# Optimization experiments

Measured on AMD Instinct MI355X. Metric: run time of the kernel, lower is better.

Reference implementation:

```python
import jax, jax.numpy as jnp
import numpy as np

N_FINE = 50000
N_COARSE = 2000
N_EDGES = 300000
HID = 512
OUT = 3
K = 3


def _gcn_prep(edge_index, n):
    # PyG GCNConv with add_self_loops=True, improved=False, edge_weight=1
    row, col = edge_index[0], edge_index[1]
    loop = jnp.arange(n, dtype=edge_index.dtype)
    row = jnp.concatenate([row, loop])
    col = jnp.concatenate([col, loop])
    deg = jax.ops.segment_sum(jnp.ones(row.shape[0], dtype=jnp.float32), col, num_segments=n)
    dis = jax.lax.rsqrt(deg)  # deg >= 1 due to self loops
    norm = dis[row] * dis[col]
    return row, col, norm


def _gcn(h, W, b, row, col, norm, n):
    # linear -> gather source -> weight by norm -> scatter-add at target -> +bias
    h = h @ W
    msg = h[row] * norm[:, None]
    return jax.ops.segment_sum(msg, col, num_segments=n) + b


def _knn_interpolate(y, coarse_pos, fine_pos, k=K):
    # squared euclidean distances [N_fine, N_coarse]
    d2 = (jnp.sum(fine_pos * fine_pos, axis=1, keepdims=True)
          + jnp.sum(coarse_pos * coarse_pos, axis=1)[None, :]
          - 2.0 * fine_pos @ coarse_pos.T)
    neg, idx = jax.lax.top_k(-d2, k)          # k nearest
    w = 1.0 / jnp.maximum(-neg, 1e-16)        # inverse squared-distance weights
    return jnp.einsum('nk,nkc->nc', w, y[idx]) / jnp.sum(w, axis=1, keepdims=True)


def setup_inputs() -> dict:
    key = jax.random.key(0)
    ks = jax.random.split(key, 20)
    x = jax.random.normal(ks[0], (N_FINE, 5), dtype=jnp.float32)
    sdf = jax.random.normal(ks[1], (N_FINE, 1), dtype=jnp.float32)
    edge_index = jax.random.randint(ks[2], (2, N_EDGES), 0, N_FINE)
    coarse_x = jax.random.normal(ks[3], (N_COARSE, 2), dtype=jnp.float32)
    coarse_y = jax.random.normal(ks[4], (N_COARSE, OUT), dtype=jnp.float32)
    dims_pre = [(6, HID), (HID, HID), (HID, HID)]
    dims_end = [(OUT + HID, HID), (HID, HID), (HID, OUT)]
    out = {"x": x, "sdf": sdf, "coarse_x": coarse_x, "coarse_y": coarse_y,
           "edge_index": edge_index}
    for i, (di, do) in enumerate(dims_pre):
        out[f"pre_W{i}"] = jax.random.normal(ks[5 + i], (di, do), dtype=jnp.float32) / np.float32(np.sqrt(di))
        out[f"pre_b{i}"] = jnp.zeros((do,), dtype=jnp.float32)
    for i, (di, do) in enumerate(dims_end):
        out[f"end_W{i}"] = jax.random.normal(ks[10 + i], (di, do), dtype=jnp.float32) / np.float32(np.sqrt(di))
        out[f"end_b{i}"] = jnp.zeros((do,), dtype=jnp.float32)
    return out


def reference(x, sdf, coarse_x, coarse_y, edge_index,
              pre_W0, pre_b0, pre_W1, pre_b1, pre_W2, pre_b2,
              end_W0, end_b0, end_W1, end_b1, end_W2, end_b2):
    n = x.shape[0]
    row, col, norm = _gcn_prep(edge_index, n)

    fine_x = jnp.concatenate([x, sdf], axis=1)  # [N, 6]
    for W, b in ((pre_W0, pre_b0), (pre_W1, pre_b1), (pre_W2, pre_b2)):
        fine_x = jax.nn.relu(_gcn(fine_x, W, b, row, col, norm, n))

    # coarse -> fine KNN upsample (batch.x[:, :2] are fine node positions)
    fine_y_orig = _knn_interpolate(coarse_y, coarse_x[:, :2], x[:, :2])  # [N, 3]

    fine_y = jnp.concatenate([fine_y_orig, fine_x], axis=1)  # [N, 515]
    for W, b in ((end_W0, end_b0), (end_W1, end_b1)):
        fine_y = jax.nn.relu(_gcn(fine_y, W, b, row, col, norm, n))
    fine_y = _gcn(fine_y, end_W2, end_b2, row, col, norm, n)
    return fine_y  # residual=False
```

## Files before the change

kernel.cpp:

```cpp
#include <hip/hip_runtime.h>
#include <hip/hip_bf16.h>

#define N_FINE 50000
#define N_COARSE 2000
#define N_EDGES 300000

typedef short  s16x8 __attribute__((ext_vector_type(8)));
typedef float  f32x4 __attribute__((ext_vector_type(4)));

static inline int cdiv(int a, int b) { return (a + b - 1) / b; }

__device__ __forceinline__ short f2b(float f) {
    unsigned u = __builtin_bit_cast(unsigned, f);
    unsigned r = (u + 0x7fffu + ((u >> 16) & 1u)) >> 16;
    return (short)r;
}
__device__ __forceinline__ float b2f(short s) {
    return __builtin_bit_cast(float, ((unsigned)(unsigned short)s) << 16);
}

#define GL16(gsrc, ldst) __builtin_amdgcn_global_load_lds( \
    (const __attribute__((address_space(1))) unsigned*)(gsrc), \
    (__attribute__((address_space(3))) unsigned*)(ldst), 16, 0, 0)


__global__ void count_edges_kernel(const int* __restrict__ col, int* __restrict__ counts, int ne) {
    int e = blockIdx.x * 256 + threadIdx.x;
    if (e < ne) atomicAdd(&counts[col[e]], 1);
}

__global__ void compute_dis_kernel(const int* __restrict__ counts, float* __restrict__ dis, int n) {
    int i = blockIdx.x * 256 + threadIdx.x;
    if (i < n) dis[i] = rsqrtf((float)(counts[i] + 1));
}

__global__ __launch_bounds__(1024) void scan_block_kernel(const int* __restrict__ counts,
        int* __restrict__ rowptr, int* __restrict__ blksum, int n) {
    __shared__ int wsum[16];
    int tid = threadIdx.x, lane = tid & 63, wv = tid >> 6;
    int i = blockIdx.x * 1024 + tid;
    int v = (i < n) ? counts[i] : 0;
    int x = v;
#pragma unroll
    for (int off = 1; off < 64; off <<= 1) {
        int t = __shfl_up(x, off);
        if (lane >= off) x += t;
    }
    if (lane == 63) wsum[wv] = x;
    __syncthreads();
    if (wv == 0) {
        int s = (lane < 16) ? wsum[lane] : 0;
#pragma unroll
        for (int off = 1; off < 16; off <<= 1) {
            int t = __shfl_up(s, off);
            if (lane >= off) s += t;
        }
        if (lane < 16) wsum[lane] = s;
    }
    __syncthreads();
    int prefix = (wv > 0) ? wsum[wv - 1] : 0;
    int incl = prefix + x;
    if (i < n) rowptr[i] = incl - v;
    if (tid == 1023) blksum[blockIdx.x] = incl;
}

__global__ void scan_tops_kernel(int* __restrict__ blksum, int nb) {
    int lane = threadIdx.x;
    int v = (lane < nb) ? blksum[lane] : 0;
    int x = v;
#pragma unroll
    for (int off = 1; off < 64; off <<= 1) {
        int t = __shfl_up(x, off);
        if (lane >= off) x += t;
    }
    if (lane < nb) blksum[lane] = x - v;
}

__global__ void scan_add_kernel(int* __restrict__ rowptr, const int* __restrict__ blksum, int n) {
    int i = blockIdx.x * 256 + threadIdx.x;
    if (i < n) rowptr[i] += blksum[i >> 10];
    else if (i == n) rowptr[n] = N_EDGES;
}

__global__ void scatter_edges_kernel(const int* __restrict__ row, const int* __restrict__ col,
                                     int* __restrict__ cursor, int* __restrict__ esrc, int ne) {
    int e = blockIdx.x * 256 + threadIdx.x;
    if (e < ne) {
        int p = atomicAdd(&cursor[col[e]], 1);
        esrc[p] = row[e];
    }
}


__global__ __launch_bounds__(256) void wt4_kernel(
        const float* __restrict__ W0, const float* __restrict__ W1,
        const float* __restrict__ W2, const float* __restrict__ W3,
        short* __restrict__ T0, short* __restrict__ T1,
        short* __restrict__ T2, short* __restrict__ T3) {
    __shared__ float tile[32][33];
    const float* W; short* WT;
    switch (blockIdx.y) {
        case 0: W = W0; WT = T0; break;
        case 1: W = W1; WT = T1; break;
        case 2: W = W2; WT = T2; break;
        default: W = W3; WT = T3; break;
    }
    int bx = blockIdx.x & 15;
    int by = blockIdx.x >> 4;
    int tx = threadIdx.x & 31;
    int ty = threadIdx.x >> 5;
#pragma unroll
    for (int i = 0; i < 4; ++i) {
        int k = bx * 32 + ty + i * 8;
        int n = by * 32 + tx;
        tile[ty + i * 8][tx] = W[(size_t)k * 512 + n];
    }
    __syncthreads();
#pragma unroll
    for (int i = 0; i < 4; ++i) {
        int n = by * 32 + ty + i * 8;
        int k = bx * 32 + tx;
        WT[(size_t)n * 512 + k] = f2b(tile[tx][ty + i * 8]);
    }
}


__global__ void pre0_kernel(const float* __restrict__ x, const float* __restrict__ sdf,
                            const float* __restrict__ W, const float* __restrict__ dis,
                            short* __restrict__ B, int M) {
    int idx = blockIdx.x * 256 + threadIdx.x;
    int m = idx >> 6, n8 = (idx & 63) << 3;
    if (m >= M) return;
    float a0 = x[m*5+0], a1 = x[m*5+1], a2 = x[m*5+2], a3 = x[m*5+3], a4 = x[m*5+4], a5 = sdf[m];
    float d = dis[m];
    s16x8 o;
#pragma unroll
    for (int j = 0; j < 8; ++j) {
        int n = n8 + j;
        float t = a0*W[n] + a1*W[512+n] + a2*W[1024+n] + a3*W[1536+n] + a4*W[2048+n] + a5*W[2560+n];
        o[j] = f2b(d * t);
    }
    *(s16x8*)&B[(size_t)m*512 + n8] = o;
}

__global__ __launch_bounds__(256) void gemm512_mfma_kernel(
        const short* __restrict__ A, const short* __restrict__ WT,
        const float* __restrict__ dis, short* __restrict__ C, int M,
        const float* __restrict__ A2, const float* __restrict__ W2) {
    __shared__ __attribute__((aligned(16))) short As[3][128 * 32];
    __shared__ __attribute__((aligned(16))) short Bs[3][128 * 32];
    int tid  = threadIdx.x;
    int lane = tid & 63;
    int w    = tid >> 6;
    int wr   = w >> 1, wc = w & 1;

    int nrp = (M + 127) >> 7;
    int id = blockIdx.x;
    int rp = (id >> 5) * 8 + (id & 7);
    int cp = (id >> 3) & 3;
    if (rp >= nrp) return;
    int row0 = rp * 128;
    int col0 = cp * 128;

    const short* aRow[2];
    const short* bRow[2];
    int ldsOff[2];
#pragma unroll
    for (int g = 0; g < 2; ++g) {
        int r = w * 32 + g * 16 + (lane >> 2);
        int ar = row0 + r; if (ar >= M) ar = M - 1;
        int sch = (lane & 3) ^ ((r >> 1) & 3);
        aRow[g] = A  + (size_t)ar * 512 + sch * 8;
        bRow[g] = WT + (size_t)(col0 + r) * 512 + sch * 8;
        ldsOff[g] = (w * 32 + g * 16) * 32;
    }

    int ks = lane >> 4;
    int aOff[4], bOff[4];
#pragma unroll
    for (int mi = 0; mi < 4; ++mi) {
        int r = wr * 64 + mi * 16 + (lane & 15);
        aOff[mi] = r * 32 + ((ks ^ ((r >> 1) & 3)) * 8);
    }
#pragma unroll
    for (int ni = 0; ni < 4; ++ni) {
        int c = wc * 64 + ni * 16 + (lane & 15);
        bOff[ni] = c * 32 + ((ks ^ ((c >> 1) & 3)) * 8);
    }

    f32x4 acc[4][4] = {};

    auto stage = [&](int buf, int k0) {
#pragma unroll
        for (int g = 0; g < 2; ++g) {
            GL16(aRow[g] + k0, &As[buf][ldsOff[g]]);
            GL16(bRow[g] + k0, &Bs[buf][ldsOff[g]]);
        }
    };
    auto compute = [&](int buf) {
        s16x8 av[4], bv[4];
#pragma unroll
        for (int mi = 0; mi < 4; ++mi) av[mi] = *(const s16x8*)&As[buf][aOff[mi]];
#pragma unroll
        for (int ni = 0; ni < 4; ++ni) bv[ni] = *(const s16x8*)&Bs[buf][bOff[ni]];
#pragma unroll
        for (int mi = 0; mi < 4; ++mi)
#pragma unroll
            for (int ni = 0; ni < 4; ++ni)
                acc[mi][ni] = __builtin_amdgcn_mfma_f32_16x16x32_bf16(av[mi], bv[ni], acc[mi][ni], 0, 0, 0);
    };

    stage(0, 0);
    stage(1, 32);
    int buf = 0;
#pragma unroll 1
    for (int t = 0; t < 16; ++t) {
        if (t + 2 < 16) {
            int b2 = buf + 2; if (b2 >= 3) b2 -= 3;
            stage(b2, (t + 2) * 32);
            asm volatile("s_waitcnt vmcnt(8)" ::: "memory");
        } else if (t + 1 < 16) {
            asm volatile("s_waitcnt vmcnt(4)" ::: "memory");
        } else {
            asm volatile("s_waitcnt vmcnt(0)" ::: "memory");
        }
        __builtin_amdgcn_s_barrier();
        __builtin_amdgcn_sched_barrier(0);
        compute(buf);
        __builtin_amdgcn_sched_barrier(0);
        __builtin_amdgcn_s_barrier();
        __builtin_amdgcn_sched_barrier(0);
        ++buf; if (buf == 3) buf = 0;
    }

    int rbase = row0 + wr * 64;
    int cbase = col0 + wc * 64;
#pragma unroll
    for (int mi = 0; mi < 4; ++mi) {
#pragma unroll
        for (int r = 0; r < 4; ++r) {
            int row = rbase + mi * 16 + (lane >> 4) * 4 + r;
            if (row >= M) continue;
            float d = dis[row];
            float a20 = 0.f, a21 = 0.f, a22 = 0.f;
            if (A2) { a20 = A2[row*3+0]; a21 = A2[row*3+1]; a22 = A2[row*3+2]; }
#pragma unroll
            for (int ni = 0; ni < 4; ++ni) {
                int col = cbase + ni * 16 + (lane & 15);
                float v = acc[mi][ni][r];
                if (A2) v += a20 * W2[col] + a21 * W2[512 + col] + a22 * W2[1024 + col];
                C[(size_t)row * 512 + col] = f2b(d * v);
            }
        }
    }
}

__global__ __launch_bounds__(256) void spmm512_kernel(
        const short* __restrict__ B, const int* __restrict__ rowptr, const int* __restrict__ esrc,
        const float* __restrict__ dis, const float* __restrict__ bias,
        short* __restrict__ out, int M) {
    int node = blockIdx.x * 4 + (threadIdx.x >> 6);
    int lane = threadIdx.x & 63;
    if (node >= M) return;
    const s16x8* Bv = (const s16x8*)B;
    s16x8 v = Bv[(size_t)node * 64 + lane];
    float acc[8];
#pragma unroll
    for (int j = 0; j < 8; ++j) acc[j] = b2f(v[j]);
    int s = rowptr[node], e = rowptr[node + 1];
    int p = s;
    for (; p + 4 <= e; p += 4) {
        int s0 = esrc[p], s1 = esrc[p+1], s2 = esrc[p+2], s3 = esrc[p+3];
        s16x8 t0 = Bv[(size_t)s0 * 64 + lane];
        s16x8 t1 = Bv[(size_t)s1 * 64 + lane];
        s16x8 t2 = Bv[(size_t)s2 * 64 + lane];
        s16x8 t3 = Bv[(size_t)s3 * 64 + lane];
#pragma unroll
        for (int j = 0; j < 8; ++j)
            acc[j] += (b2f(t0[j]) + b2f(t1[j])) + (b2f(t2[j]) + b2f(t3[j]));
    }
    for (; p < e; ++p) {
        int src = esrc[p];
        s16x8 t = Bv[(size_t)src * 64 + lane];
#pragma unroll
        for (int j = 0; j < 8; ++j) acc[j] += b2f(t[j]);
    }
    float d = dis[node];
    const float4* bp = (const float4*)bias;
    float4 bb0 = bp[lane * 2], bb1 = bp[lane * 2 + 1];
    float r[8];
    r[0] = d*acc[0] + bb0.x; r[1] = d*acc[1] + bb0.y; r[2] = d*acc[2] + bb0.z; r[3] = d*acc[3] + bb0.w;
    r[4] = d*acc[4] + bb1.x; r[5] = d*acc[5] + bb1.y; r[6] = d*acc[6] + bb1.z; r[7] = d*acc[7] + bb1.w;
    s16x8 o;
#pragma unroll
    for (int j = 0; j < 8; ++j) o[j] = f2b(fmaxf(r[j], 0.f));
    ((s16x8*)out)[(size_t)node * 64 + lane] = o;
}

__global__ __launch_bounds__(256) void gemm_n3_kernel(
        const short* __restrict__ A, const float* __restrict__ W,
        const float* __restrict__ dis, float* __restrict__ B3, int M) {
    int wid = (blockIdx.x * 256 + threadIdx.x) >> 6;
    int lane = threadIdx.x & 63;
    if (wid >= M) return;
    s16x8 v = ((const s16x8*)A)[(size_t)wid * 64 + lane];
    float s0 = 0.f, s1 = 0.f, s2 = 0.f;
#pragma unroll
    for (int j = 0; j < 8; ++j) {
        float a = b2f(v[j]);
        int k = lane * 8 + j;
        s0 += a * W[k*3+0];
        s1 += a * W[k*3+1];
        s2 += a * W[k*3+2];
    }
    for (int off = 32; off > 0; off >>= 1) {
        s0 += __shfl_down(s0, off);
        s1 += __shfl_down(s1, off);
        s2 += __shfl_down(s2, off);
    }
    if (lane == 0) {
        float d = dis[wid];
        B3[wid*3+0] = d * s0;
        B3[wid*3+1] = d * s1;
        B3[wid*3+2] = d * s2;
    }
}

__global__ void spmm3_kernel(const float* __restrict__ B3, const int* __restrict__ rowptr,
                             const int* __restrict__ esrc, const float* __restrict__ dis,
                             const float* __restrict__ bias, float* __restrict__ out, int M) {
    int i = blockIdx.x * 256 + threadIdx.x;
    if (i >= M) return;
    float a0 = B3[i*3+0], a1 = B3[i*3+1], a2 = B3[i*3+2];
    int s = rowptr[i], e = rowptr[i + 1];
    for (int p = s; p < e; ++p) {
        int src = esrc[p];
        a0 += B3[src*3+0];
        a1 += B3[src*3+1];
        a2 += B3[src*3+2];
    }
    float d = dis[i];
    out[i*3+0] = d * a0 + bias[0];
    out[i*3+1] = d * a1 + bias[1];
    out[i*3+2] = d * a2 + bias[2];
}

__global__ __launch_bounds__(256) void knn_kernel(
        const float* __restrict__ x, const float* __restrict__ cpos,
        const float* __restrict__ cy, float* __restrict__ fy, int M) {
    __shared__ float sd[12][64];
    __shared__ int   si[12][64];
    int lane = threadIdx.x & 63;
    int w = threadIdx.x >> 6;
    int gi = blockIdx.x * 64 + lane;
    int i = (gi < M) ? gi : (M - 1);
    float px = x[i*5+0], py = x[i*5+1];
    float pn2 = px*px + py*py;
    float d0 = 3.0e38f, d1 = 3.0e38f, d2 = 3.0e38f;
    int i0 = 0x7fffffff, i1 = 0x7fffffff, i2 = 0x7fffffff;
    int c0 = w * (N_COARSE / 4), c1 = c0 + (N_COARSE / 4);
    for (int c = c0; c < c1; ++c) {
        float a = cpos[c*2+0], b = cpos[c*2+1];
        float sn2 = a*a + b*b;
        float d = pn2 + sn2 - 2.f * (px * a + py * b);
        if (d < d2) {
            if (d < d1) {
                d2 = d1; i2 = i1;
                if (d < d0) { d1 = d0; i1 = i0; d0 = d; i0 = c; }
                else       { d1 = d;  i1 = c; }
            } else { d2 = d; i2 = c; }
        }
    }
    sd[w*3+0][lane] = d0; si[w*3+0][lane] = i0;
    sd[w*3+1][lane] = d1; si[w*3+1][lane] = i1;
    sd[w*3+2][lane] = d2; si[w*3+2][lane] = i2;
    __syncthreads();
    if (w != 0 || gi >= M) return;
    float cd[12]; int ci[12];
#pragma unroll
    for (int q = 0; q < 12; ++q) { cd[q] = sd[q][lane]; ci[q] = si[q][lane]; }
    float bd[3]; int bi[3];
#pragma unroll
    for (int s = 0; s < 3; ++s) {
        float best = 3.4e38f; int besti = 0x7fffffff; int bq = 0;
#pragma unroll
        for (int q = 0; q < 12; ++q) {
            bool better = (cd[q] < best) || (cd[q] == best && ci[q] < besti);
            if (better) { best = cd[q]; besti = ci[q]; bq = q; }
        }
        bd[s] = best; bi[s] = besti;
        cd[bq] = 3.4e38f; ci[bq] = 0x7fffffff;
    }
    float w0 = 1.f / fmaxf(bd[0], 1e-16f);
    float w1 = 1.f / fmaxf(bd[1], 1e-16f);
    float w2 = 1.f / fmaxf(bd[2], 1e-16f);
    float ws = w0 + w1 + w2;
    int j0 = bi[0], j1 = bi[1], j2 = bi[2];
#pragma unroll
    for (int j = 0; j < 3; ++j) {
        float v = w0 * cy[j0*3+j] + w1 * cy[j1*3+j] + w2 * cy[j2*3+j];
        fy[gi*3+j] = v / ws;
    }
}


extern "C" void kernel_launch(void* const* d_in, const int* in_sizes, int n_in,
                              void* d_out, int out_size, void* d_ws, size_t ws_size,
                              hipStream_t stream) {
    const float* x        = (const float*)d_in[0];
    const float* sdf      = (const float*)d_in[1];
    const float* coarse_x = (const float*)d_in[2];
    const float* coarse_y = (const float*)d_in[3];
    const int*   eidx     = (const int*)d_in[4];
    const float* pre_W0   = (const float*)d_in[5];
    const float* pre_b0   = (const float*)d_in[6];
    const float* pre_W1   = (const float*)d_in[7];
    const float* pre_b1   = (const float*)d_in[8];
    const float* pre_W2   = (const float*)d_in[9];
    const float* pre_b2   = (const float*)d_in[10];
    const float* end_W0   = (const float*)d_in[11];
    const float* end_b0   = (const float*)d_in[12];
    const float* end_W1   = (const float*)d_in[13];
    const float* end_b1   = (const float*)d_in[14];
    const float* end_W2   = (const float*)d_in[15];
    const float* end_b2   = (const float*)d_in[16];
    float* out = (float*)d_out;

    const int M = N_FINE, NE = N_EDGES;
    const int* erow = eidx;
    const int* ecol = eidx + NE;

    char* base = (char*)d_ws;
    size_t off = 0;
    auto alloc = [&](size_t bytes) { char* p = base + off; off = (off + bytes + 255) & ~(size_t)255; return p; };
    int*   counts = (int*)  alloc((size_t)M * 4);
    int*   rowptr = (int*)  alloc((size_t)(M + 1) * 4);
    int*   cursor = (int*)  alloc((size_t)M * 4);
    int*   esrc   = (int*)  alloc((size_t)NE * 4);
    int*   blksum = (int*)  alloc((size_t)64 * 4);
    float* dis    = (float*)alloc((size_t)M * 4);
    float* fy     = (float*)alloc((size_t)M * 3 * 4);
    float* B3     = (float*)alloc((size_t)M * 3 * 4);
    short* WT1    = (short*)alloc((size_t)512 * 512 * 2);
    short* WT2    = (short*)alloc((size_t)512 * 512 * 2);
    short* WT3    = (short*)alloc((size_t)512 * 512 * 2);
    short* WT4    = (short*)alloc((size_t)512 * 512 * 2);
    short* bufA   = (short*)alloc((size_t)M * 512 * 2);
    short* bufB   = (short*)alloc((size_t)M * 512 * 2);
    (void)ws_size;

    wt4_kernel<<<dim3(256, 4), 256, 0, stream>>>(pre_W1, pre_W2, end_W0 + 3 * 512, end_W1,
                                                 WT1, WT2, WT3, WT4);

    hipMemsetAsync(counts, 0, (size_t)M * 4, stream);
    count_edges_kernel<<<cdiv(NE, 256), 256, 0, stream>>>(ecol, counts, NE);
    compute_dis_kernel<<<cdiv(M, 256), 256, 0, stream>>>(counts, dis, M);
    int nb = cdiv(M, 1024);
    scan_block_kernel<<<nb, 1024, 0, stream>>>(counts, rowptr, blksum, M);
    scan_tops_kernel<<<1, 64, 0, stream>>>(blksum, nb);
    scan_add_kernel<<<cdiv(M + 1, 256), 256, 0, stream>>>(rowptr, blksum, M);
    hipMemcpyAsync(cursor, rowptr, (size_t)M * 4, hipMemcpyDeviceToDevice, stream);
    scatter_edges_kernel<<<cdiv(NE, 256), 256, 0, stream>>>(erow, ecol, cursor, esrc, NE);

    knn_kernel<<<cdiv(M, 64), 256, 0, stream>>>(x, coarse_x, coarse_y, fy, M);

    int nrp = cdiv(M, 128);
    int ggrid = cdiv(nrp, 8) * 32;
    int sgrid = cdiv(M, 4);

    pre0_kernel<<<cdiv(M * 64, 256), 256, 0, stream>>>(x, sdf, pre_W0, dis, bufB, M);
    spmm512_kernel<<<sgrid, 256, 0, stream>>>(bufB, rowptr, esrc, dis, pre_b0, bufA, M);

    gemm512_mfma_kernel<<<ggrid, 256, 0, stream>>>(bufA, WT1, dis, bufB, M, nullptr, nullptr);
    spmm512_kernel<<<sgrid, 256, 0, stream>>>(bufB, rowptr, esrc, dis, pre_b1, bufA, M);

    gemm512_mfma_kernel<<<ggrid, 256, 0, stream>>>(bufA, WT2, dis, bufB, M, nullptr, nullptr);
    spmm512_kernel<<<sgrid, 256, 0, stream>>>(bufB, rowptr, esrc, dis, pre_b2, bufA, M);

    gemm512_mfma_kernel<<<ggrid, 256, 0, stream>>>(bufA, WT3, dis, bufB, M, fy, end_W0);
    spmm512_kernel<<<sgrid, 256, 0, stream>>>(bufB, rowptr, esrc, dis, end_b0, bufA, M);

    gemm512_mfma_kernel<<<ggrid, 256, 0, stream>>>(bufA, WT4, dis, bufB, M, nullptr, nullptr);
    spmm512_kernel<<<sgrid, 256, 0, stream>>>(bufB, rowptr, esrc, dis, end_b1, bufA, M);

    gemm_n3_kernel<<<cdiv(M * 64, 256), 256, 0, stream>>>(bufA, end_W2, dis, B3, M);
    spmm3_kernel<<<cdiv(M, 256), 256, 0, stream>>>(B3, rowptr, esrc, dis, end_b2, out, M);
}
```

Measured before the change: 680.2 us.

## Enlarge MFMA GEMM tile to 256x128 with 8 waves and BK=64 pipeline

The 512-wide bf16 GEMM now uses 512-thread blocks computing 256x128 output tiles with a K-step of 64. The A tile is triple-buffered and the B tile double-buffered in LDS, with an XOR swizzle adapted to 64-wide rows. Global-to-LDS loads for the next steps are issued between the two K-halves of each step, and the MFMA bursts are wrapped in s_setprio. This raises per-block data reuse and overlaps loads with compute, at the cost of about 128 KB of LDS per block, which limits occupancy to one block per CU.

```diff
diff --git a/kernel.cpp b/kernel.cpp
--- a/kernel.cpp
+++ b/kernel.cpp
@@ -143,98 +143,113 @@
     *(s16x8*)&B[(size_t)m*512 + n8] = o;
 }
 
-__global__ __launch_bounds__(256) void gemm512_mfma_kernel(
+__global__ __launch_bounds__(512) void gemm512_mfma_kernel(
         const short* __restrict__ A, const short* __restrict__ WT,
         const float* __restrict__ dis, short* __restrict__ C, int M,
         const float* __restrict__ A2, const float* __restrict__ W2) {
-    __shared__ __attribute__((aligned(16))) short As[3][128 * 32];
-    __shared__ __attribute__((aligned(16))) short Bs[3][128 * 32];
+    __shared__ __attribute__((aligned(16))) short As[3 * 256 * 64];
+    __shared__ __attribute__((aligned(16))) short Bs[2 * 128 * 64];
     int tid  = threadIdx.x;
     int lane = tid & 63;
     int w    = tid >> 6;
-    int wr   = w >> 1, wc = w & 1;
-
-    int nrp = (M + 127) >> 7;
+    int wm   = w >> 1, wn = w & 1;
+
+    int nrp = (M + 255) >> 8;
     int id = blockIdx.x;
     int rp = (id >> 5) * 8 + (id & 7);
     int cp = (id >> 3) & 3;
     if (rp >= nrp) return;
-    int row0 = rp * 128;
+    int row0 = rp * 256;
     int col0 = cp * 128;
 
-    const short* aRow[2];
-    const short* bRow[2];
-    int ldsOff[2];
-#pragma unroll
-    for (int g = 0; g < 2; ++g) {
-        int r = w * 32 + g * 16 + (lane >> 2);
-        int ar = row0 + r; if (ar >= M) ar = M - 1;
-        int sch = (lane & 3) ^ ((r >> 1) & 3);
-        aRow[g] = A  + (size_t)ar * 512 + sch * 8;
-        bRow[g] = WT + (size_t)(col0 + r) * 512 + sch * 8;
-        ldsOff[g] = (w * 32 + g * 16) * 32;
-    }
-
-    int ks = lane >> 4;
-    int aOff[4], bOff[4];
-#pragma unroll
-    for (int mi = 0; mi < 4; ++mi) {
-        int r = wr * 64 + mi * 16 + (lane & 15);
-        aOff[mi] = r * 32 + ((ks ^ ((r >> 1) & 3)) * 8);
-    }
-#pragma unroll
-    for (int ni = 0; ni < 4; ++ni) {
-        int c = wc * 64 + ni * 16 + (lane & 15);
-        bOff[ni] = c * 32 + ((ks ^ ((c >> 1) & 3)) * 8);
+    int sch = ((lane & 7) ^ (lane >> 3)) * 8;
+    const short* aS[2][2];
+    int aD[2][2];
+#pragma unroll
+    for (int h = 0; h < 2; ++h)
+#pragma unroll
+        for (int s = 0; s < 2; ++s) {
+            int rbase = h * 128 + s * 64 + w * 8;
+            int gr = row0 + rbase + (lane >> 3); if (gr >= M) gr = M - 1;
+            aS[h][s] = A + (size_t)gr * 512 + sch;
+            aD[h][s] = rbase * 64;
+        }
+    const short* bS[2];
+    int bD[2];
+#pragma unroll
+    for (int h = 0; h < 2; ++h) {
+        int rbase = h * 64 + w * 8;
+        bS[h] = WT + (size_t)(col0 + rbase + (lane >> 3)) * 512 + sch;
+        bD[h] = rbase * 64;
+    }
+
+    int aOff[2][4], bOff[2][4];
+#pragma unroll
+    for (int p = 0; p < 2; ++p) {
+        int c = ((p * 4 + (lane >> 4)) ^ (lane & 7)) * 8;
+#pragma unroll
+        for (int mi = 0; mi < 4; ++mi)
+            aOff[p][mi] = (wm * 64 + mi * 16 + (lane & 15)) * 64 + c;
+#pragma unroll
+        for (int ni = 0; ni < 4; ++ni)
+            bOff[p][ni] = (wn * 64 + ni * 16 + (lane & 15)) * 64 + c;
     }
 
     f32x4 acc[4][4] = {};
 
-    auto stage = [&](int buf, int k0) {
-#pragma unroll
-        for (int g = 0; g < 2; ++g) {
-            GL16(aRow[g] + k0, &As[buf][ldsOff[g]]);
-            GL16(bRow[g] + k0, &Bs[buf][ldsOff[g]]);
-        }
+    auto stageA = [&](int bf, int k0, int h) {
+        GL16(aS[h][0] + k0, &As[bf * 16384 + aD[h][0]]);
+        GL16(aS[h][1] + k0, &As[bf * 16384 + aD[h][1]]);
     };
-    auto compute = [&](int buf) {
-        s16x8 av[4], bv[4];
-#pragma unroll
-        for (int mi = 0; mi < 4; ++mi) av[mi] = *(const s16x8*)&As[buf][aOff[mi]];
-#pragma unroll
-        for (int ni = 0; ni < 4; ++ni) bv[ni] = *(const s16x8*)&Bs[buf][bOff[ni]];
-#pragma unroll
-        for (int mi = 0; mi < 4; ++mi)
-#pragma unroll
-            for (int ni = 0; ni < 4; ++ni)
-                acc[mi][ni] = __builtin_amdgcn_mfma_f32_16x16x32_bf16(av[mi], bv[ni], acc[mi][ni], 0, 0, 0);
+    auto stageB = [&](int bf, int k0) {
+        GL16(bS[0] + k0, &Bs[bf * 8192 + bD[0]]);
+        GL16(bS[1] + k0, &Bs[bf * 8192 + bD[1]]);
     };
 
-    stage(0, 0);
-    stage(1, 32);
-    int buf = 0;
+    stageA(0, 0, 0); stageA(0, 0, 1);
+    stageB(0, 0);
+    stageA(1, 64, 0); stageA(1, 64, 1);
+
 #pragma unroll 1
-    for (int t = 0; t < 16; ++t) {
-        if (t + 2 < 16) {
-            int b2 = buf + 2; if (b2 >= 3) b2 -= 3;
-            stage(b2, (t + 2) * 32);
-            asm volatile("s_waitcnt vmcnt(8)" ::: "memory");
-        } else if (t + 1 < 16) {
-            asm volatile("s_waitcnt vmcnt(4)" ::: "memory");
-        } else {
-            asm volatile("s_waitcnt vmcnt(0)" ::: "memory");
-        }
+    for (int kt = 0; kt < 8; ++kt) {
+        int abuf = kt % 3;
+        int bbuf = kt & 1;
+        int a2buf = (kt + 2) % 3;
+        if (kt == 7) { asm volatile("s_waitcnt vmcnt(0)" ::: "memory"); }
+        else         { asm volatile("s_waitcnt vmcnt(4)" ::: "memory"); }
         __builtin_amdgcn_s_barrier();
         __builtin_amdgcn_sched_barrier(0);
-        compute(buf);
-        __builtin_amdgcn_sched_barrier(0);
-        __builtin_amdgcn_s_barrier();
-        __builtin_amdgcn_sched_barrier(0);
-        ++buf; if (buf == 3) buf = 0;
-    }
-
-    int rbase = row0 + wr * 64;
-    int cbase = col0 + wc * 64;
+#pragma unroll
+        for (int p = 0; p < 2; ++p) {
+            s16x8 av[4], bv[4];
+#pragma unroll
+            for (int mi = 0; mi < 4; ++mi) av[mi] = *(const s16x8*)&As[abuf * 16384 + aOff[p][mi]];
+#pragma unroll
+            for (int ni = 0; ni < 4; ++ni) bv[ni] = *(const s16x8*)&Bs[bbuf * 8192 + bOff[p][ni]];
+            if (p == 0) {
+                if (kt + 1 < 8) stageB((kt + 1) & 1, (kt + 1) * 64);
+                if (kt + 2 < 8) stageA(a2buf, (kt + 2) * 64, 0);
+            } else {
+                if (kt + 2 < 8) stageA(a2buf, (kt + 2) * 64, 1);
+            }
+            __builtin_amdgcn_s_barrier();
+            __builtin_amdgcn_sched_barrier(0);
+            asm volatile("s_waitcnt lgkmcnt(0)" ::: "memory");
+            __builtin_amdgcn_sched_barrier(0);
+            __builtin_amdgcn_s_setprio(1);
+#pragma unroll
+            for (int mi = 0; mi < 4; ++mi)
+#pragma unroll
+                for (int ni = 0; ni < 4; ++ni)
+                    acc[mi][ni] = __builtin_amdgcn_mfma_f32_16x16x32_bf16(av[mi], bv[ni], acc[mi][ni], 0, 0, 0);
+            __builtin_amdgcn_s_setprio(0);
+            __builtin_amdgcn_s_barrier();
+            __builtin_amdgcn_sched_barrier(0);
+        }
+    }
+
+    int rbase = row0 + wm * 64;
+    int cbase = col0 + wn * 64;
 #pragma unroll
     for (int mi = 0; mi < 4; ++mi) {
 #pragma unroll
@@ -464,23 +479,23 @@
 
     knn_kernel<<<cdiv(M, 64), 256, 0, stream>>>(x, coarse_x, coarse_y, fy, M);
 
-    int nrp = cdiv(M, 128);
+    int nrp = cdiv(M, 256);
     int ggrid = cdiv(nrp, 8) * 32;
     int sgrid = cdiv(M, 4);
 
     pre0_kernel<<<cdiv(M * 64, 256), 256, 0, stream>>>(x, sdf, pre_W0, dis, bufB, M);
     spmm512_kernel<<<sgrid, 256, 0, stream>>>(bufB, rowptr, esrc, dis, pre_b0, bufA, M);
 
-    gemm512_mfma_kernel<<<ggrid, 256, 0, stream>>>(bufA, WT1, dis, bufB, M, nullptr, nullptr);
+    gemm512_mfma_kernel<<<ggrid, 512, 0, stream>>>(bufA, WT1, dis, bufB, M, nullptr, nullptr);
     spmm512_kernel<<<sgrid, 256, 0, stream>>>(bufB, rowptr, esrc, dis, pre_b1, bufA, M);
 
-    gemm512_mfma_kernel<<<ggrid, 256, 0, stream>>>(bufA, WT2, dis, bufB, M, nullptr, nullptr);
+    gemm512_mfma_kernel<<<ggrid, 512, 0, stream>>>(bufA, WT2, dis, bufB, M, nullptr, nullptr);
     spmm512_kernel<<<sgrid, 256, 0, stream>>>(bufB, rowptr, esrc, dis, pre_b2, bufA, M);
 
-    gemm512_mfma_kernel<<<ggrid, 256, 0, stream>>>(bufA, WT3, dis, bufB, M, fy, end_W0);
+    gemm512_mfma_kernel<<<ggrid, 512, 0, stream>>>(bufA, WT3, dis, bufB, M, fy, end_W0);
     spmm512_kernel<<<sgrid, 256, 0, stream>>>(bufB, rowptr, esrc, dis, end_b0, bufA, M);
 
-    gemm512_mfma_kernel<<<ggrid, 256, 0, stream>>>(bufA, WT4, dis, bufB, M, nullptr, nullptr);
+    gemm512_mfma_kernel<<<ggrid, 512, 0, stream>>>(bufA, WT4, dis, bufB, M, nullptr, nullptr);
     spmm512_kernel<<<sgrid, 256, 0, stream>>>(bufB, rowptr, esrc, dis, end_b1, bufA, M);
 
     gemm_n3_kernel<<<cdiv(M * 64, 256), 256, 0, stream>>>(bufA, end_W2, dis, B3, M);
```

New measurement: 711.6 us. 1.05x slower.

## Load GEMM operands directly from global into registers, dropping LDS staging

Applied to the files above, without the earlier changes.

Removes the triple-buffered LDS staging (global_load_lds plus barriers) from the 512-wide bf16 MFMA GEMM. Each wave now loads its A and B fragments straight from global memory into registers, with one-step register double buffering. This eliminates LDS traffic and block barriers. In exchange, each wave loads its own data, so fragments shared between waves are fetched twice from global/L2, and the loads are less coalesced (16-byte chunks spread across 16 rows).

```diff
diff --git a/kernel.cpp b/kernel.cpp
--- a/kernel.cpp
+++ b/kernel.cpp
@@ -18,10 +18,6 @@
 __device__ __forceinline__ float b2f(short s) {
     return __builtin_bit_cast(float, ((unsigned)(unsigned short)s) << 16);
 }
-
-#define GL16(gsrc, ldst) __builtin_amdgcn_global_load_lds( \
-    (const __attribute__((address_space(1))) unsigned*)(gsrc), \
-    (__attribute__((address_space(3))) unsigned*)(ldst), 16, 0, 0)
 
 
 __global__ void count_edges_kernel(const int* __restrict__ col, int* __restrict__ counts, int ne) {
@@ -147,12 +143,10 @@
         const short* __restrict__ A, const short* __restrict__ WT,
         const float* __restrict__ dis, short* __restrict__ C, int M,
         const float* __restrict__ A2, const float* __restrict__ W2) {
-    __shared__ __attribute__((aligned(16))) short As[3][128 * 32];
-    __shared__ __attribute__((aligned(16))) short Bs[3][128 * 32];
     int tid  = threadIdx.x;
     int lane = tid & 63;
     int w    = tid >> 6;
-    int wr   = w >> 1, wc = w & 1;
+    int wm   = w >> 1, wn = w & 1;
 
     int nrp = (M + 127) >> 7;
     int id = blockIdx.x;
@@ -162,79 +156,64 @@
     int row0 = rp * 128;
     int col0 = cp * 128;
 
-    const short* aRow[2];
-    const short* bRow[2];
-    int ldsOff[2];
-#pragma unroll
-    for (int g = 0; g < 2; ++g) {
-        int r = w * 32 + g * 16 + (lane >> 2);
-        int ar = row0 + r; if (ar >= M) ar = M - 1;
-        int sch = (lane & 3) ^ ((r >> 1) & 3);
-        aRow[g] = A  + (size_t)ar * 512 + sch * 8;
-        bRow[g] = WT + (size_t)(col0 + r) * 512 + sch * 8;
-        ldsOff[g] = (w * 32 + g * 16) * 32;
-    }
-
-    int ks = lane >> 4;
-    int aOff[4], bOff[4];
+    int r16 = lane & 15;
+    int kc  = lane >> 4;
+
+    const short* pA[4];
+    const short* pB[4];
 #pragma unroll
     for (int mi = 0; mi < 4; ++mi) {
-        int r = wr * 64 + mi * 16 + (lane & 15);
-        aOff[mi] = r * 32 + ((ks ^ ((r >> 1) & 3)) * 8);
+        int ar = row0 + wm * 64 + mi * 16 + r16; if (ar >= M) ar = M - 1;
+        pA[mi] = A + (size_t)ar * 512 + kc * 8;
     }
 #pragma unroll
     for (int ni = 0; ni < 4; ++ni) {
-        int c = wc * 64 + ni * 16 + (lane & 15);
-        bOff[ni] = c * 32 + ((ks ^ ((c >> 1) & 3)) * 8);
+        int br = col0 + wn * 64 + ni * 16 + r16;
+        pB[ni] = WT + (size_t)br * 512 + kc * 8;
     }
 
     f32x4 acc[4][4] = {};
-
-    auto stage = [&](int buf, int k0) {
-#pragma unroll
-        for (int g = 0; g < 2; ++g) {
-            GL16(aRow[g] + k0, &As[buf][ldsOff[g]]);
-            GL16(bRow[g] + k0, &Bs[buf][ldsOff[g]]);
-        }
-    };
-    auto compute = [&](int buf) {
-        s16x8 av[4], bv[4];
-#pragma unroll
-        for (int mi = 0; mi < 4; ++mi) av[mi] = *(const s16x8*)&As[buf][aOff[mi]];
-#pragma unroll
-        for (int ni = 0; ni < 4; ++ni) bv[ni] = *(const s16x8*)&Bs[buf][bOff[ni]];
-#pragma unroll
-        for (int mi = 0; mi < 4; ++mi)
-#pragma unroll
-            for (int ni = 0; ni < 4; ++ni)
-                acc[mi][ni] = __builtin_amdgcn_mfma_f32_16x16x32_bf16(av[mi], bv[ni], acc[mi][ni], 0, 0, 0);
-    };
-
-    stage(0, 0);
-    stage(1, 32);
-    int buf = 0;
+    s16x8 a0, a1, a2, a3, b0, b1, b2, b3;
+    s16x8 na0, na1, na2, na3, nb0, nb1, nb2, nb3;
+
+    a0 = *(const s16x8*)pA[0]; a1 = *(const s16x8*)pA[1];
+    a2 = *(const s16x8*)pA[2]; a3 = *(const s16x8*)pA[3];
+    b0 = *(const s16x8*)pB[0]; b1 = *(const s16x8*)pB[1];
+    b2 = *(const s16x8*)pB[2]; b3 = *(const s16x8*)pB[3];
+
 #pragma unroll 1
     for (int t = 0; t < 16; ++t) {
-        if (t + 2 < 16) {
-            int b2 = buf + 2; if (b2 >= 3) b2 -= 3;
-            stage(b2, (t + 2) * 32);
-            asm volatile("s_waitcnt vmcnt(8)" ::: "memory");
-        } else if (t + 1 < 16) {
-            asm volatile("s_waitcnt vmcnt(4)" ::: "memory");
-        } else {
-            asm volatile("s_waitcnt vmcnt(0)" ::: "memory");
-        }
-        __builtin_amdgcn_s_barrier();
-        __builtin_amdgcn_sched_barrier(0);
-        compute(buf);
-        __builtin_amdgcn_sched_barrier(0);
-        __builtin_amdgcn_s_barrier();
-        __builtin_amdgcn_sched_barrier(0);
-        ++buf; if (buf == 3) buf = 0;
-    }
-
-    int rbase = row0 + wr * 64;
-    int cbase = col0 + wc * 64;
+        if (t < 15) {
+            int ko = (t + 1) * 32;
+            na0 = *(const s16x8*)(pA[0] + ko); na1 = *(const s16x8*)(pA[1] + ko);
+            na2 = *(const s16x8*)(pA[2] + ko); na3 = *(const s16x8*)(pA[3] + ko);
+            nb0 = *(const s16x8*)(pB[0] + ko); nb1 = *(const s16x8*)(pB[1] + ko);
+            nb2 = *(const s16x8*)(pB[2] + ko); nb3 = *(const s16x8*)(pB[3] + ko);
+        }
+        acc[0][0] = __builtin_amdgcn_mfma_f32_16x16x32_bf16(a0, b0, acc[0][0], 0, 0, 0);
+        acc[0][1] = __builtin_amdgcn_mfma_f32_16x16x32_bf16(a0, b1, acc[0][1], 0, 0, 0);
+        acc[0][2] = __builtin_amdgcn_mfma_f32_16x16x32_bf16(a0, b2, acc[0][2], 0, 0, 0);
+        acc[0][3] = __builtin_amdgcn_mfma_f32_16x16x32_bf16(a0, b3, acc[0][3], 0, 0, 0);
+        acc[1][0] = __builtin_amdgcn_mfma_f32_16x16x32_bf16(a1, b0, acc[1][0], 0, 0, 0);
+        acc[1][1] = __builtin_amdgcn_mfma_f32_16x16x32_bf16(a1, b1, acc[1][1], 0, 0, 0);
+        acc[1][2] = __builtin_amdgcn_mfma_f32_16x16x32_bf16(a1, b2, acc[1][2], 0, 0, 0);
+        acc[1][3] = __builtin_amdgcn_mfma_f32_16x16x32_bf16(a1, b3, acc[1][3], 0, 0, 0);
+        acc[2][0] = __builtin_amdgcn_mfma_f32_16x16x32_bf16(a2, b0, acc[2][0], 0, 0, 0);
+        acc[2][1] = __builtin_amdgcn_mfma_f32_16x16x32_bf16(a2, b1, acc[2][1], 0, 0, 0);
+        acc[2][2] = __builtin_amdgcn_mfma_f32_16x16x32_bf16(a2, b2, acc[2][2], 0, 0, 0);
+        acc[2][3] = __builtin_amdgcn_mfma_f32_16x16x32_bf16(a2, b3, acc[2][3], 0, 0, 0);
+        acc[3][0] = __builtin_amdgcn_mfma_f32_16x16x32_bf16(a3, b0, acc[3][0], 0, 0, 0);
+        acc[3][1] = __builtin_amdgcn_mfma_f32_16x16x32_bf16(a3, b1, acc[3][1], 0, 0, 0);
+        acc[3][2] = __builtin_amdgcn_mfma_f32_16x16x32_bf16(a3, b2, acc[3][2], 0, 0, 0);
+        acc[3][3] = __builtin_amdgcn_mfma_f32_16x16x32_bf16(a3, b3, acc[3][3], 0, 0, 0);
+        if (t < 15) {
+            a0 = na0; a1 = na1; a2 = na2; a3 = na3;
+            b0 = nb0; b1 = nb1; b2 = nb2; b3 = nb3;
+        }
+    }
+
+    int rbase = row0 + wm * 64;
+    int cbase = col0 + wn * 64;
 #pragma unroll
     for (int mi = 0; mi < 4; ++mi) {
 #pragma unroll
```

Result: slower. 949.2 us (+39.6%).

## Enlarge GEMM tile to 256x128 with 8 waves and K-step 64

Applied to the files above, without the earlier changes.

The dense 512-wide GEMM now uses 512-thread blocks covering 256 rows by 128 columns, with a K step of 64 per stage. The LDS swizzle is reworked for 64-element rows. The larger tile cuts the number of blocks and the redundant reloads of the weight tile, and halves the number of loop iterations and barriers. In exchange it needs more LDS (about 147 KB for triple buffering), which lowers occupancy to one block per CU and leaves fewer blocks to spread across the CUs.

```diff
diff --git a/kernel.cpp b/kernel.cpp
--- a/kernel.cpp
+++ b/kernel.cpp
@@ -143,84 +143,95 @@
     *(s16x8*)&B[(size_t)m*512 + n8] = o;
 }
 
-__global__ __launch_bounds__(256) void gemm512_mfma_kernel(
+__global__ __launch_bounds__(512) void gemm512_mfma_kernel(
         const short* __restrict__ A, const short* __restrict__ WT,
         const float* __restrict__ dis, short* __restrict__ C, int M,
         const float* __restrict__ A2, const float* __restrict__ W2) {
-    __shared__ __attribute__((aligned(16))) short As[3][128 * 32];
-    __shared__ __attribute__((aligned(16))) short Bs[3][128 * 32];
+    __shared__ __attribute__((aligned(16))) short As[3 * 256 * 64];
+    __shared__ __attribute__((aligned(16))) short Bs[3 * 128 * 64];
     int tid  = threadIdx.x;
     int lane = tid & 63;
     int w    = tid >> 6;
-    int wr   = w >> 1, wc = w & 1;
-
-    int nrp = (M + 127) >> 7;
+    int wm   = w >> 1, wn = w & 1;
+
+    int nrp = (M + 255) >> 8;
     int id = blockIdx.x;
     int rp = (id >> 5) * 8 + (id & 7);
     int cp = (id >> 3) & 3;
     if (rp >= nrp) return;
-    int row0 = rp * 128;
+    int row0 = rp * 256;
     int col0 = cp * 128;
 
-    const short* aRow[2];
+    const short* aRow[4];
+    int aOffD[4];
+#pragma unroll
+    for (int g = 0; g < 4; ++g) {
+        int r = w * 32 + g * 8 + (lane >> 3);
+        int gr = row0 + r; if (gr >= M) gr = M - 1;
+        int sch = (lane & 7) ^ (r & 7);
+        aRow[g] = A + (size_t)gr * 512 + sch * 8;
+        aOffD[g] = (w * 32 + g * 8) * 64;
+    }
     const short* bRow[2];
-    int ldsOff[2];
+    int bOffD[2];
 #pragma unroll
     for (int g = 0; g < 2; ++g) {
-        int r = w * 32 + g * 16 + (lane >> 2);
-        int ar = row0 + r; if (ar >= M) ar = M - 1;
-        int sch = (lane & 3) ^ ((r >> 1) & 3);
-        aRow[g] = A  + (size_t)ar * 512 + sch * 8;
+        int r = w * 16 + g * 8 + (lane >> 3);
+        int sch = (lane & 7) ^ (r & 7);
         bRow[g] = WT + (size_t)(col0 + r) * 512 + sch * 8;
-        ldsOff[g] = (w * 32 + g * 16) * 32;
-    }
-
-    int ks = lane >> 4;
-    int aOff[4], bOff[4];
-#pragma unroll
-    for (int mi = 0; mi < 4; ++mi) {
-        int r = wr * 64 + mi * 16 + (lane & 15);
-        aOff[mi] = r * 32 + ((ks ^ ((r >> 1) & 3)) * 8);
-    }
-#pragma unroll
-    for (int ni = 0; ni < 4; ++ni) {
-        int c = wc * 64 + ni * 16 + (lane & 15);
-        bOff[ni] = c * 32 + ((ks ^ ((c >> 1) & 3)) * 8);
+        bOffD[g] = (w * 16 + g * 8) * 64;
+    }
+
+    int aOff[2][4], bOff[2][4];
+#pragma unroll
+    for (int p = 0; p < 2; ++p) {
+#pragma unroll
+        for (int mi = 0; mi < 4; ++mi) {
+            int r = wm * 64 + mi * 16 + (lane & 15);
+            aOff[p][mi] = r * 64 + (((p * 4 + (lane >> 4)) ^ (r & 7)) * 8);
+        }
+#pragma unroll
+        for (int ni = 0; ni < 4; ++ni) {
+            int c = wn * 64 + ni * 16 + (lane & 15);
+            bOff[p][ni] = c * 64 + (((p * 4 + (lane >> 4)) ^ (c & 7)) * 8);
+        }
     }
 
     f32x4 acc[4][4] = {};
 
     auto stage = [&](int buf, int k0) {
 #pragma unroll
-        for (int g = 0; g < 2; ++g) {
-            GL16(aRow[g] + k0, &As[buf][ldsOff[g]]);
-            GL16(bRow[g] + k0, &Bs[buf][ldsOff[g]]);
-        }
+        for (int g = 0; g < 4; ++g) GL16(aRow[g] + k0, &As[buf * 16384 + aOffD[g]]);
+#pragma unroll
+        for (int g = 0; g < 2; ++g) GL16(bRow[g] + k0, &Bs[buf * 8192 + bOffD[g]]);
     };
     auto compute = [&](int buf) {
-        s16x8 av[4], bv[4];
-#pragma unroll
-        for (int mi = 0; mi < 4; ++mi) av[mi] = *(const s16x8*)&As[buf][aOff[mi]];
-#pragma unroll
-        for (int ni = 0; ni < 4; ++ni) bv[ni] = *(const s16x8*)&Bs[buf][bOff[ni]];
-#pragma unroll
-        for (int mi = 0; mi < 4; ++mi)
-#pragma unroll
-            for (int ni = 0; ni < 4; ++ni)
-                acc[mi][ni] = __builtin_amdgcn_mfma_f32_16x16x32_bf16(av[mi], bv[ni], acc[mi][ni], 0, 0, 0);
+#pragma unroll
+        for (int p = 0; p < 2; ++p) {
+            s16x8 av[4], bv[4];
+#pragma unroll
+            for (int mi = 0; mi < 4; ++mi) av[mi] = *(const s16x8*)&As[buf * 16384 + aOff[p][mi]];
+#pragma unroll
+            for (int ni = 0; ni < 4; ++ni) bv[ni] = *(const s16x8*)&Bs[buf * 8192 + bOff[p][ni]];
+#pragma unroll
+            for (int mi = 0; mi < 4; ++mi)
+#pragma unroll
+                for (int ni = 0; ni < 4; ++ni)
+                    acc[mi][ni] = __builtin_amdgcn_mfma_f32_16x16x32_bf16(av[mi], bv[ni], acc[mi][ni], 0, 0, 0);
+        }
     };
 
     stage(0, 0);
-    stage(1, 32);
+    stage(1, 64);
     int buf = 0;
 #pragma unroll 1
-    for (int t = 0; t < 16; ++t) {
-        if (t + 2 < 16) {
+    for (int t = 0; t < 8; ++t) {
+        if (t + 2 < 8) {
             int b2 = buf + 2; if (b2 >= 3) b2 -= 3;
-            stage(b2, (t + 2) * 32);
-            asm volatile("s_waitcnt vmcnt(8)" ::: "memory");
-        } else if (t + 1 < 16) {
-            asm volatile("s_waitcnt vmcnt(4)" ::: "memory");
+            stage(b2, (t + 2) * 64);
+            asm volatile("s_waitcnt vmcnt(12)" ::: "memory");
+        } else if (t + 1 < 8) {
+            asm volatile("s_waitcnt vmcnt(6)" ::: "memory");
         } else {
             asm volatile("s_waitcnt vmcnt(0)" ::: "memory");
         }
@@ -233,8 +244,8 @@
         ++buf; if (buf == 3) buf = 0;
     }
 
-    int rbase = row0 + wr * 64;
-    int cbase = col0 + wc * 64;
+    int rbase = row0 + wm * 64;
+    int cbase = col0 + wn * 64;
 #pragma unroll
     for (int mi = 0; mi < 4; ++mi) {
 #pragma unroll
@@ -464,23 +475,23 @@
 
     knn_kernel<<<cdiv(M, 64), 256, 0, stream>>>(x, coarse_x, coarse_y, fy, M);
 
-    int nrp = cdiv(M, 128);
+    int nrp = cdiv(M, 256);
     int ggrid = cdiv(nrp, 8) * 32;
     int sgrid = cdiv(M, 4);
 
     pre0_kernel<<<cdiv(M * 64, 256), 256, 0, stream>>>(x, sdf, pre_W0, dis, bufB, M);
     spmm512_kernel<<<sgrid, 256, 0, stream>>>(bufB, rowptr, esrc, dis, pre_b0, bufA, M);
 
-    gemm512_mfma_kernel<<<ggrid, 256, 0, stream>>>(bufA, WT1, dis, bufB, M, nullptr, nullptr);
+    gemm512_mfma_kernel<<<ggrid, 512, 0, stream>>>(bufA, WT1, dis, bufB, M, nullptr, nullptr);
     spmm512_kernel<<<sgrid, 256, 0, stream>>>(bufB, rowptr, esrc, dis, pre_b1, bufA, M);
 
-    gemm512_mfma_kernel<<<ggrid, 256, 0, stream>>>(bufA, WT2, dis, bufB, M, nullptr, nullptr);
+    gemm512_mfma_kernel<<<ggrid, 512, 0, stream>>>(bufA, WT2, dis, bufB, M, nullptr, nullptr);
     spmm512_kernel<<<sgrid, 256, 0, stream>>>(bufB, rowptr, esrc, dis, pre_b2, bufA, M);
 
-    gemm512_mfma_kernel<<<ggrid, 256, 0, stream>>>(bufA, WT3, dis, bufB, M, fy, end_W0);
+    gemm512_mfma_kernel<<<ggrid, 512, 0, stream>>>(bufA, WT3, dis, bufB, M, fy, end_W0);
     spmm512_kernel<<<sgrid, 256, 0, stream>>>(bufB, rowptr, esrc, dis, end_b0, bufA, M);
 
-    gemm512_mfma_kernel<<<ggrid, 256, 0, stream>>>(bufA, WT4, dis, bufB, M, nullptr, nullptr);
+    gemm512_mfma_kernel<<<ggrid, 512, 0, stream>>>(bufA, WT4, dis, bufB, M, nullptr, nullptr);
     spmm512_kernel<<<sgrid, 256, 0, stream>>>(bufB, rowptr, esrc, dis, end_b1, bufA, M);
 
     gemm_n3_kernel<<<cdiv(M * 64, 256), 256, 0, stream>>>(bufA, end_W2, dis, B3, M);
```

After: 724.0 us. +6.4%, slower.
